# Performance work log

Hardware: AMD Instinct MI355X
Metric: run time of the kernel (lower is better)

The kernel has to match this reference:

```python
import jax, jax.numpy as jnp
import numpy as np

N, T, CIN, COUT, H, W = 8, 20, 32, 64, 64, 64
K, PAD, POOL = 3, 1, 2
EPS = 1e-5  # torch BatchNorm2d default eps (used only in the ANN/BN path, as in source)


def _conv2d(x, w, b):
    # x: (B, Cin, H, W), w: (Cout, Cin, kH, kW)
    y = jax.lax.conv_general_dilated(
        x, w, window_strides=(1, 1), padding=[(PAD, PAD), (PAD, PAD)],
        dimension_numbers=("NCHW", "OIHW", "NCHW"))
    return y + b[None, :, None, None]


def _maxpool(x, p):
    return jax.lax.reduce_window(x, -jnp.inf, jax.lax.max,
                                 (1, 1, p, p), (1, 1, p, p), "VALID")


@jax.custom_vjp
def _spike(pot, mask):
    # actF.forward: spike = (pot >= 1).float() * (1 - spike_mask)
    return (pot >= 1.0).astype(pot.dtype) * (1.0 - mask)


def _spike_fwd(pot, mask):
    s = (pot >= 1.0).astype(pot.dtype) * (1.0 - mask)
    return s, s


def _spike_bwd(s, g):
    # actF.backward: grad_pot = grad_out * (-spike); grad for mask is None
    return (g * (-s), jnp.zeros_like(s))


_spike.defvjp(_spike_fwd, _spike_bwd)


def setup_inputs() -> dict:
    key = jax.random.key(0)
    ks = jax.random.split(key, 8)
    fan_in = CIN * K * K
    return {
        "input_feature_st": jax.random.normal(ks[0], (N, T, CIN, H, W), jnp.float32),
        "input_features_sc": jax.random.normal(ks[1], (N, CIN, H, W), jnp.float32),
        "conv_w": jax.random.normal(ks[2], (COUT, CIN, K, K), jnp.float32) / np.sqrt(fan_in),
        "conv_b": jax.random.normal(ks[3], (COUT,), jnp.float32) * 0.1,
        "gamma": jax.random.normal(ks[4], (COUT,), jnp.float32) * 2.0,  # nn.init.normal_(bn.weight, 0, weight_init=2.0)
        "beta": jax.random.normal(ks[5], (COUT,), jnp.float32) * 0.1,
        "running_mean": jax.random.normal(ks[6], (COUT,), jnp.float32) * 0.1,
        "running_var": jax.random.uniform(ks[7], (COUT,), jnp.float32, 0.5, 1.5),
    }


def _forward(x_st, x_sc, w, b, gamma, beta, rm, rv):
    rm = jax.lax.stop_gradient(rm)  # BN buffers carry no grad in torch
    rv = jax.lax.stop_gradient(rv)
    # --- ANN path: conv -> BN(eval, running stats) -> maxpool -> relu ---
    y = _conv2d(x_sc, w, b)
    scale = (gamma / jnp.sqrt(rv + EPS))[None, :, None, None]
    y = (y - rm[None, :, None, None]) * scale + beta[None, :, None, None]
    ann_output = jax.nn.relu(_maxpool(y, POOL))
    # --- BN-folded spiking path (conv weight/bias detached, as in source) ---
    ratio = gamma / jnp.sqrt(rv)  # NOTE: no eps, matching source exactly
    wN = jax.lax.stop_gradient(w) * ratio[:, None, None, None]
    bN = (jax.lax.stop_gradient(b) - rm) * ratio + beta
    n, t = x_st.shape[0], x_st.shape[1]
    xt = x_st.reshape((n * t,) + x_st.shape[2:])
    pooled = _maxpool(_conv2d(xt, wN, bN), POOL)            # (N*T, Cout, OH, OW)
    pooled = pooled.reshape((n, t) + pooled.shape[1:])
    pooled = jnp.transpose(pooled, (1, 0, 2, 3, 4))          # (T, N, Cout, OH, OW)
    pot0 = jnp.zeros_like(pooled[0])
    mask0 = jnp.zeros_like(pooled[0])

    def step(carry, p_t):
        pot, mask = carry
        pot = pot + p_t
        s = _spike(pot, mask)
        pot = pot - s
        mask = (mask + s > 0).astype(pot.dtype)  # spike_mask += s; spike_mask[>0]=1
        return (pot, mask), s

    _, spikes = jax.lax.scan(step, (pot0, mask0), pooled)    # (T, N, Cout, OH, OW)
    spike_out = jnp.transpose(spikes, (1, 0, 2, 3, 4))       # (N, T, Cout, OH, OW)
    spike_count_out = spike_out.sum(axis=1)
    return spike_out, spike_count_out, ann_output


def reference(input_feature_st, input_features_sc, conv_w, conv_b, gamma, beta, running_mean, running_var):
    return _forward(input_feature_st, input_features_sc, conv_w, conv_b,
                    gamma, beta, running_mean, running_var)
```

## Files before the change

### kernel.cpp

```cpp
#include <hip/hip_runtime.h>

namespace {
constexpr int T = 20;
constexpr int CINc = 32;
constexpr int COUTc = 64;
constexpr int HWc = 64;
constexpr int IMG = CINc * HWc * HWc;
constexpr int OHW = 32;
constexpr int PLANE = OHW * OHW;
constexpr int SPIKE_SZ = 8 * T * COUTc * PLANE;
constexpr int CNT_SZ = 8 * COUTc * PLANE;
constexpr int W_ELEMS = 9 * COUTc * CINc;
constexpr float LO_SCALE = 16777216.0f;
constexpr float LO_INV = 5.9604644775390625e-8f;
}

typedef _Float16 half8 __attribute__((ext_vector_type(8)));
typedef float f32x4 __attribute__((ext_vector_type(4)));

__device__ __forceinline__ unsigned short h_bits(_Float16 h) {
  return __builtin_bit_cast(unsigned short, h);
}

__global__ void wprep_kernel(const float* __restrict__ w,
                             const float* __restrict__ gamma,
                             const float* __restrict__ rv,
                             unsigned short* __restrict__ ws) {
  int idx = blockIdx.x * 256 + threadIdx.x;
  if (idx >= 2 * W_ELEMS) return;
  int ci = idx & 31;
  int co = (idx >> 5) & 63;
  int v = idx >> 11;
  int tap = v % 9;
  int set = v / 9;
  float denom = set ? sqrtf(rv[co] + 1e-5f) : sqrtf(rv[co]);
  float val = w[(co * 32 + ci) * 9 + tap] * (gamma[co] / denom);
  _Float16 h = (_Float16)val;
  _Float16 l = (_Float16)((val - (float)h) * LO_SCALE);
  int base = set * (2 * W_ELEMS) + (tap * 64 + co) * 32 + ci;
  ws[base] = h_bits(h);
  ws[base + W_ELEMS] = h_bits(l);
}

__global__ __launch_bounds__(256, 2)
void conv_mfma_kernel(const float* __restrict__ x_st,
                      const float* __restrict__ x_sc,
                      const float* __restrict__ b,
                      const float* __restrict__ gamma,
                      const float* __restrict__ beta,
                      const float* __restrict__ rm,
                      const float* __restrict__ rv,
                      const unsigned short* __restrict__ ws,
                      float* __restrict__ out) {
  __shared__ unsigned short in_h[6 * 66 * 32];
  __shared__ unsigned short in_l[6 * 66 * 32];

  const int tid = threadIdx.x;
  const int band = blockIdx.x;
  const int job = blockIdx.y;
  const bool spiking = job < 160;
  const int r0 = band * 4;

  const float* __restrict__ xin =
      spiking ? (x_st + (size_t)job * IMG) : (x_sc + (size_t)(job - 160) * IMG);

  {
    const int col = tid & 63;
    const int g = tid >> 6;
    for (int r6 = 0; r6 < 6; ++r6) {
      int row = r0 - 1 + r6;
      float vv[8];
      if ((unsigned)row < 64u) {
        const float* src = xin + (g * 8) * (HWc * HWc) + row * HWc + col;
        #pragma unroll
        for (int jj = 0; jj < 8; ++jj) vv[jj] = src[jj * (HWc * HWc)];
      } else {
        #pragma unroll
        for (int jj = 0; jj < 8; ++jj) vv[jj] = 0.f;
      }
      unsigned int hw[4], lw[4];
      #pragma unroll
      for (int q = 0; q < 4; ++q) {
        float x0 = vv[2 * q], x1 = vv[2 * q + 1];
        _Float16 h0 = (_Float16)x0;
        _Float16 h1 = (_Float16)x1;
        _Float16 l0 = (_Float16)((x0 - (float)h0) * LO_SCALE);
        _Float16 l1 = (_Float16)((x1 - (float)h1) * LO_SCALE);
        hw[q] = (unsigned int)h_bits(h0) | ((unsigned int)h_bits(h1) << 16);
        lw[q] = (unsigned int)h_bits(l0) | ((unsigned int)h_bits(l1) << 16);
      }
      int base = (r6 * 66 + col + 1) * 32 + g * 8;
      *reinterpret_cast<uint4*>(&in_h[base]) = make_uint4(hw[0], hw[1], hw[2], hw[3]);
      *reinterpret_cast<uint4*>(&in_l[base]) = make_uint4(lw[0], lw[1], lw[2], lw[3]);
    }
    if (tid < 12) {
      int r6 = tid >> 1;
      int slot = (tid & 1) * 65;
      int base = (r6 * 66 + slot) * 32;
      uint4 z = make_uint4(0, 0, 0, 0);
      #pragma unroll
      for (int q = 0; q < 4; ++q) {
        *reinterpret_cast<uint4*>(&in_h[base + q * 8]) = z;
        *reinterpret_cast<uint4*>(&in_l[base + q * 8]) = z;
      }
    }
  }
  __syncthreads();

  const int lane = tid & 63;
  const int wv = tid >> 6;
  const int p = wv & 1;
  const int co0 = (wv >> 1) * 32;
  const int laneoff = (lane & 15) * 64 + (lane >> 4) * 16;

  const char* Hbase = (const char*)in_h;
  const char* Lbase = (const char*)in_l;
  const char* WS = (const char*)ws + (spiking ? 0 : 4 * W_ELEMS);
  const int WLO = 2 * W_ELEMS;

  f32x4 accH[8][2];
  f32x4 accL[8][2];
  #pragma unroll
  for (int m = 0; m < 8; ++m) {
    accH[m][0] = (f32x4)(0.f);
    accH[m][1] = (f32x4)(0.f);
    accL[m][0] = (f32x4)(0.f);
    accL[m][1] = (f32x4)(0.f);
  }

  #pragma unroll
  for (int ky = 0; ky < 3; ++ky) {
    #pragma unroll
    for (int kx = 0; kx < 3; ++kx) {
      const int tap = ky * 3 + kx;
      const char* wp = WS + (tap * 64 + co0) * 64 + laneoff;
      half8 bh0 = *reinterpret_cast<const half8*>(wp);
      half8 bh1 = *reinterpret_cast<const half8*>(wp + 16 * 64);
      half8 bl0 = *reinterpret_cast<const half8*>(wp + WLO);
      half8 bl1 = *reinterpret_cast<const half8*>(wp + WLO + 16 * 64);
      #pragma unroll
      for (int m = 0; m < 8; ++m) {
        const int rl = 2 * p + (m >> 2) + ky;
        const int boff = (rl * 66 + (m & 3) * 16 + kx) * 64;
        half8 ah = *reinterpret_cast<const half8*>(Hbase + boff + laneoff);
        half8 al = *reinterpret_cast<const half8*>(Lbase + boff + laneoff);
        accH[m][0] = __builtin_amdgcn_mfma_f32_16x16x32_f16(ah, bh0, accH[m][0], 0, 0, 0);
        accH[m][1] = __builtin_amdgcn_mfma_f32_16x16x32_f16(ah, bh1, accH[m][1], 0, 0, 0);
        accL[m][0] = __builtin_amdgcn_mfma_f32_16x16x32_f16(al, bh0, accL[m][0], 0, 0, 0);
        accL[m][0] = __builtin_amdgcn_mfma_f32_16x16x32_f16(ah, bl0, accL[m][0], 0, 0, 0);
        accL[m][1] = __builtin_amdgcn_mfma_f32_16x16x32_f16(al, bh1, accL[m][1], 0, 0, 0);
        accL[m][1] = __builtin_amdgcn_mfma_f32_16x16x32_f16(ah, bl1, accL[m][1], 0, 0, 0);
      }
    }
  }

  const int oy = band * 2 + p;
  #pragma unroll
  for (int j = 0; j < 2; ++j) {
    int co = co0 + j * 16 + (lane & 15);
    float denom = spiking ? sqrtf(rv[co]) : sqrtf(rv[co] + 1e-5f);
    float rs = gamma[co] / denom;
    float beff = (b[co] - rm[co]) * rs + beta[co];
    #pragma unroll
    for (int m = 0; m < 4; ++m) {
      f32x4 tH = accH[m][j], tL = accL[m][j];
      f32x4 bH = accH[m + 4][j], bL = accL[m + 4][j];
      float t0 = fmaf(LO_INV, tL[0], tH[0]);
      float t1 = fmaf(LO_INV, tL[1], tH[1]);
      float t2 = fmaf(LO_INV, tL[2], tH[2]);
      float t3 = fmaf(LO_INV, tL[3], tH[3]);
      float b0 = fmaf(LO_INV, bL[0], bH[0]);
      float b1 = fmaf(LO_INV, bL[1], bH[1]);
      float b2 = fmaf(LO_INV, bL[2], bH[2]);
      float b3 = fmaf(LO_INV, bL[3], bH[3]);
      float v0 = fmaxf(fmaxf(t0, t1), fmaxf(b0, b1)) + beff;
      float v1 = fmaxf(fmaxf(t2, t3), fmaxf(b2, b3)) + beff;
      int ox = m * 8 + (lane >> 4) * 2;
      if (spiking) {
        float2* dst = reinterpret_cast<float2*>(
            out + (size_t)(job * COUTc + co) * PLANE + oy * OHW + ox);
        *dst = make_float2(v0, v1);
      } else {
        int n = job - 160;
        float2* dst = reinterpret_cast<float2*>(
            out + (size_t)(SPIKE_SZ + CNT_SZ) +
            (size_t)(n * COUTc + co) * PLANE + oy * OHW + ox);
        *dst = make_float2(fmaxf(v0, 0.f), fmaxf(v1, 0.f));
      }
    }
  }
}

__global__ __launch_bounds__(256)
void scan_kernel(float* __restrict__ out) {
  int g = blockIdx.x * 256 + threadIdx.x;
  int n = g >> 16;
  int rem = g & 65535;
  size_t base = (size_t)n * (T * COUTc * PLANE) + rem;
  float pot = 0.f;
  float spiked = 0.f;
  #pragma unroll
  for (int t = 0; t < T; ++t) {
    size_t idx = base + (size_t)t * (COUTc * PLANE);
    float v = out[idx];
    pot += v;
    float s = (pot >= 1.f && spiked == 0.f) ? 1.f : 0.f;
    out[idx] = s;
    pot -= s;
    spiked = fmaxf(spiked, s);
  }
  out[(size_t)SPIKE_SZ + g] = spiked;
}

extern "C" void kernel_launch(void* const* d_in, const int* in_sizes, int n_in,
                              void* d_out, int out_size, void* d_ws, size_t ws_size,
                              hipStream_t stream) {
  const float* x_st  = (const float*)d_in[0];
  const float* x_sc  = (const float*)d_in[1];
  const float* w     = (const float*)d_in[2];
  const float* b     = (const float*)d_in[3];
  const float* gamma = (const float*)d_in[4];
  const float* beta  = (const float*)d_in[5];
  const float* rm    = (const float*)d_in[6];
  const float* rv    = (const float*)d_in[7];
  float* out = (float*)d_out;
  unsigned short* wsu = (unsigned short*)d_ws;

  wprep_kernel<<<(2 * W_ELEMS + 255) / 256, 256, 0, stream>>>(w, gamma, rv, wsu);
  dim3 grid(16, 168);
  conv_mfma_kernel<<<grid, 256, 0, stream>>>(x_st, x_sc, b, gamma, beta, rm, rv, wsu, out);
  scan_kernel<<<2048, 256, 0, stream>>>(out);
}
```

Measured before the change: 100.9 us.

## Split conv accumulation into two row phases, swizzle LDS, raise occupancy

The MFMA accumulation over 8 row-tiles is split into two sequential phases of 4 row-tiles each, with the partial 2x2 max-pool folded into a small running-max array. This halves live accumulator registers, so launch bounds can ask for 3 blocks per SIMD instead of 2. The LDS input tile layout also gets an XOR swizzle on the 16-byte chunk index to reduce bank conflicts on the half8 reads. The cost is that the weight fragments are reloaded in each phase and there is less instruction-level parallelism per wave.

```diff
diff --git a/kernel.cpp b/kernel.cpp
--- a/kernel.cpp
+++ b/kernel.cpp
@@ -42,7 +42,7 @@
   ws[base + W_ELEMS] = h_bits(l);
 }
 
-__global__ __launch_bounds__(256, 2)
+__global__ __launch_bounds__(256, 3)
 void conv_mfma_kernel(const float* __restrict__ x_st,
                       const float* __restrict__ x_sc,
                       const float* __restrict__ b,
@@ -89,9 +89,10 @@
         hw[q] = (unsigned int)h_bits(h0) | ((unsigned int)h_bits(h1) << 16);
         lw[q] = (unsigned int)h_bits(l0) | ((unsigned int)h_bits(l1) << 16);
       }
-      int base = (r6 * 66 + col + 1) * 32 + g * 8;
-      *reinterpret_cast<uint4*>(&in_h[base]) = make_uint4(hw[0], hw[1], hw[2], hw[3]);
-      *reinterpret_cast<uint4*>(&in_l[base]) = make_uint4(lw[0], lw[1], lw[2], lw[3]);
+      int lin = ((r6 * 66 + col + 1) * 4 + g) * 16;
+      int sw = lin ^ ((lin & 0x180) >> 3);
+      *reinterpret_cast<uint4*>((char*)in_h + sw) = make_uint4(hw[0], hw[1], hw[2], hw[3]);
+      *reinterpret_cast<uint4*>((char*)in_l + sw) = make_uint4(lw[0], lw[1], lw[2], lw[3]);
     }
     if (tid < 12) {
       int r6 = tid >> 1;
@@ -118,38 +119,65 @@
   const char* WS = (const char*)ws + (spiking ? 0 : 4 * W_ELEMS);
   const int WLO = 2 * W_ELEMS;
 
-  f32x4 accH[8][2];
-  f32x4 accL[8][2];
+  float hp[4][2][2];
   #pragma unroll
-  for (int m = 0; m < 8; ++m) {
-    accH[m][0] = (f32x4)(0.f);
-    accH[m][1] = (f32x4)(0.f);
-    accL[m][0] = (f32x4)(0.f);
-    accL[m][1] = (f32x4)(0.f);
-  }
-
-  #pragma unroll
-  for (int ky = 0; ky < 3; ++ky) {
-    #pragma unroll
-    for (int kx = 0; kx < 3; ++kx) {
-      const int tap = ky * 3 + kx;
-      const char* wp = WS + (tap * 64 + co0) * 64 + laneoff;
-      half8 bh0 = *reinterpret_cast<const half8*>(wp);
-      half8 bh1 = *reinterpret_cast<const half8*>(wp + 16 * 64);
-      half8 bl0 = *reinterpret_cast<const half8*>(wp + WLO);
-      half8 bl1 = *reinterpret_cast<const half8*>(wp + WLO + 16 * 64);
-      #pragma unroll
-      for (int m = 0; m < 8; ++m) {
-        const int rl = 2 * p + (m >> 2) + ky;
-        const int boff = (rl * 66 + (m & 3) * 16 + kx) * 64;
-        half8 ah = *reinterpret_cast<const half8*>(Hbase + boff + laneoff);
-        half8 al = *reinterpret_cast<const half8*>(Lbase + boff + laneoff);
-        accH[m][0] = __builtin_amdgcn_mfma_f32_16x16x32_f16(ah, bh0, accH[m][0], 0, 0, 0);
-        accH[m][1] = __builtin_amdgcn_mfma_f32_16x16x32_f16(ah, bh1, accH[m][1], 0, 0, 0);
-        accL[m][0] = __builtin_amdgcn_mfma_f32_16x16x32_f16(al, bh0, accL[m][0], 0, 0, 0);
-        accL[m][0] = __builtin_amdgcn_mfma_f32_16x16x32_f16(ah, bl0, accL[m][0], 0, 0, 0);
-        accL[m][1] = __builtin_amdgcn_mfma_f32_16x16x32_f16(al, bh1, accL[m][1], 0, 0, 0);
-        accL[m][1] = __builtin_amdgcn_mfma_f32_16x16x32_f16(ah, bl1, accL[m][1], 0, 0, 0);
+  for (int m = 0; m < 4; ++m)
+    #pragma unroll
+    for (int j = 0; j < 2; ++j) {
+      hp[m][j][0] = -__builtin_inff();
+      hp[m][j][1] = -__builtin_inff();
+    }
+
+  #pragma unroll 1
+  for (int phase = 0; phase < 2; ++phase) {
+    f32x4 accH[4][2];
+    f32x4 accL[4][2];
+    #pragma unroll
+    for (int m = 0; m < 4; ++m) {
+      accH[m][0] = (f32x4)(0.f);
+      accH[m][1] = (f32x4)(0.f);
+      accL[m][0] = (f32x4)(0.f);
+      accL[m][1] = (f32x4)(0.f);
+    }
+
+    #pragma unroll
+    for (int ky = 0; ky < 3; ++ky) {
+      #pragma unroll
+      for (int kx = 0; kx < 3; ++kx) {
+        const int tap = ky * 3 + kx;
+        const char* wp = WS + (tap * 64 + co0) * 64 + laneoff;
+        half8 bh0 = *reinterpret_cast<const half8*>(wp);
+        half8 bh1 = *reinterpret_cast<const half8*>(wp + 16 * 64);
+        half8 bl0 = *reinterpret_cast<const half8*>(wp + WLO);
+        half8 bl1 = *reinterpret_cast<const half8*>(wp + WLO + 16 * 64);
+        const int r6idx = 2 * p + phase + ky;
+        #pragma unroll
+        for (int m = 0; m < 4; ++m) {
+          int lin = (r6idx * 66 + m * 16 + kx) * 64 + laneoff;
+          int sw = lin ^ ((lin & 0x180) >> 3);
+          half8 ah = *reinterpret_cast<const half8*>(Hbase + sw);
+          half8 al = *reinterpret_cast<const half8*>(Lbase + sw);
+          accH[m][0] = __builtin_amdgcn_mfma_f32_16x16x32_f16(ah, bh0, accH[m][0], 0, 0, 0);
+          accH[m][1] = __builtin_amdgcn_mfma_f32_16x16x32_f16(ah, bh1, accH[m][1], 0, 0, 0);
+          accL[m][0] = __builtin_amdgcn_mfma_f32_16x16x32_f16(al, bh0, accL[m][0], 0, 0, 0);
+          accL[m][0] = __builtin_amdgcn_mfma_f32_16x16x32_f16(ah, bl0, accL[m][0], 0, 0, 0);
+          accL[m][1] = __builtin_amdgcn_mfma_f32_16x16x32_f16(al, bh1, accL[m][1], 0, 0, 0);
+          accL[m][1] = __builtin_amdgcn_mfma_f32_16x16x32_f16(ah, bl1, accL[m][1], 0, 0, 0);
+        }
+      }
+    }
+
+    #pragma unroll
+    for (int m = 0; m < 4; ++m) {
+      #pragma unroll
+      for (int j = 0; j < 2; ++j) {
+        f32x4 tH = accH[m][j], tL = accL[m][j];
+        float t0 = fmaf(LO_INV, tL[0], tH[0]);
+        float t1 = fmaf(LO_INV, tL[1], tH[1]);
+        float t2 = fmaf(LO_INV, tL[2], tH[2]);
+        float t3 = fmaf(LO_INV, tL[3], tH[3]);
+        hp[m][j][0] = fmaxf(hp[m][j][0], fmaxf(t0, t1));
+        hp[m][j][1] = fmaxf(hp[m][j][1], fmaxf(t2, t3));
       }
     }
   }
@@ -163,18 +191,8 @@
     float beff = (b[co] - rm[co]) * rs + beta[co];
     #pragma unroll
     for (int m = 0; m < 4; ++m) {
-      f32x4 tH = accH[m][j], tL = accL[m][j];
-      f32x4 bH = accH[m + 4][j], bL = accL[m + 4][j];
-      float t0 = fmaf(LO_INV, tL[0], tH[0]);
-      float t1 = fmaf(LO_INV, tL[1], tH[1]);
-      float t2 = fmaf(LO_INV, tL[2], tH[2]);
-      float t3 = fmaf(LO_INV, tL[3], tH[3]);
-      float b0 = fmaf(LO_INV, bL[0], bH[0]);
-      float b1 = fmaf(LO_INV, bL[1], bH[1]);
-      float b2 = fmaf(LO_INV, bL[2], bH[2]);
-      float b3 = fmaf(LO_INV, bL[3], bH[3]);
-      float v0 = fmaxf(fmaxf(t0, t1), fmaxf(b0, b1)) + beff;
-      float v1 = fmaxf(fmaxf(t2, t3), fmaxf(b2, b3)) + beff;
+      float v0 = hp[m][j][0] + beff;
+      float v1 = hp[m][j][1] + beff;
       int ox = m * 8 + (lane >> 4) * 2;
       if (spiking) {
         float2* dst = reinterpret_cast<float2*>(
```

After: 171.7 us. 1.7x slower.
